# Optimization experiments

Hardware: AMD Instinct MI355X
Metric: run time of the kernel (lower is better)

The kernel has to match this reference:

```python
import jax, jax.numpy as jnp
import numpy as np

DIM = 8          # per-head dim
ATT_EPS = 1e-15
BN_EPS = 1e-6


def setup_inputs() -> dict:
    key = jax.random.key(0)
    ks = jax.random.split(key, 6)
    B, C, H, W = 8, 256, 64, 64
    td = 256                      # heads * dim = 32 * 8
    return {
        'x':      jax.random.normal(ks[0], (B, C, H, W), jnp.float32),
        'w_qkv':  jax.random.normal(ks[1], (3 * td, C), jnp.float32) * 0.05,
        'w_dw':   jax.random.normal(ks[2], (3 * td, 1, 5, 5), jnp.float32) * 0.05,
        'w_pw':   jax.random.normal(ks[3], (96, 8, 8), jnp.float32) * 0.05,   # (groups, out/g, in/g)
        'w_proj': jax.random.normal(ks[4], (C, 2 * td), jnp.float32) * 0.05,
        'bn_gamma': jnp.ones((C,), jnp.float32),
        'bn_beta':  jnp.zeros((C,), jnp.float32),
        'bn_mean':  jnp.zeros((C,), jnp.float32),
        'bn_var':   jnp.ones((C,), jnp.float32),
    }


def _relu_linear_att(ms, H, W):
    # ms: [B, C, H, W] with C = heads * 3*DIM
    B = ms.shape[0]
    d = DIM
    qkv = ms.reshape(B, -1, 3 * d, H * W).transpose(0, 1, 3, 2)   # [B, h, N, 3d]
    q = jax.nn.relu(qkv[..., :d])
    k = jax.nn.relu(qkv[..., d:2 * d])
    v = qkv[..., 2 * d:]
    v = jnp.pad(v, ((0, 0), (0, 0), (0, 0), (0, 1)), constant_values=1.0)  # ones column
    kv = jnp.einsum('bhnd,bhne->bhde', k, v)                       # [B, h, d, d+1]
    out = jnp.einsum('bhnd,bhde->bhne', q, kv)                     # [B, h, N, d+1]
    out = out[..., :-1] / (out[..., -1:] + ATT_EPS)
    return out.transpose(0, 1, 3, 2).reshape(B, -1, H, W)          # [B, h*d, H, W]


def reference(x, w_qkv, w_dw, w_pw, w_proj, bn_gamma, bn_beta, bn_mean, bn_var):
    B, C, H, W = x.shape
    # 1x1 qkv projection
    qkv = jnp.einsum('oc,bchw->bohw', w_qkv, x)                    # [B, 768, H, W]
    # multiscale aggregation: 5x5 depthwise then grouped 1x1 (groups = 3*heads = 96)
    dw = jax.lax.conv_general_dilated(
        qkv, w_dw, window_strides=(1, 1), padding=[(2, 2), (2, 2)],
        dimension_numbers=('NCHW', 'OIHW', 'NCHW'),
        feature_group_count=qkv.shape[1])
    G, O, I = w_pw.shape
    agg = jnp.einsum('goi,bgihw->bgohw', w_pw,
                     dw.reshape(B, G, I, H, W)).reshape(B, G * O, H, W)
    ms = jnp.concatenate([qkv, agg], axis=1)                       # [B, 1536, H, W]
    att = _relu_linear_att(ms, H, W)                               # [B, 512, H, W]
    # proj: 1x1 conv + BatchNorm (eval mode) + identity activation
    p = jnp.einsum('oc,bchw->bohw', w_proj, att)                   # [B, 256, H, W]
    inv = bn_gamma / jnp.sqrt(bn_var + BN_EPS)
    p = p * inv[None, :, None, None] + (bn_beta - bn_mean * inv)[None, :, None, None]
    return x + p
```

## Files before the change

### kernel.cpp

```cpp
#include <hip/hip_runtime.h>
#include <hip/hip_bf16.h>


#define HW 4096
#define ATT_EPS 1e-15f
#define BN_EPS 1e-6f

typedef __attribute__((ext_vector_type(8))) short short8;
typedef __attribute__((ext_vector_type(4))) short short4v;
typedef __attribute__((ext_vector_type(4))) float f32x4;
typedef __attribute__((ext_vector_type(2))) float f32x2;
typedef __attribute__((ext_vector_type(8))) unsigned short u16x8;
typedef __attribute__((ext_vector_type(4))) unsigned short u16x4;

static __device__ inline short f2bf(float f) {
    union { float f; unsigned u; } v; v.f = f;
    unsigned r = v.u + 0x7fff + ((v.u >> 16) & 1);
    return (short)(r >> 16);
}
static __device__ inline float bf2f(unsigned short u) {
    union { unsigned u; float f; } v; v.u = (unsigned)u << 16; return v.f;
}

__global__ __launch_bounds__(256) void prep_w(const float* __restrict__ wproj,
                                              unsigned short* __restrict__ wbf) {
    const int i = (blockIdx.x * 256 + threadIdx.x) * 4;
    float4 v = *(const float4*)&wproj[i];
    u16x4 r = {(unsigned short)f2bf(v.x), (unsigned short)f2bf(v.y),
               (unsigned short)f2bf(v.z), (unsigned short)f2bf(v.w)};
    *(u16x4*)&wbf[i] = r;
}

__global__ __launch_bounds__(256) void qkv_gemm(const float* __restrict__ x,
                                                const float* __restrict__ w,
                                                unsigned short* __restrict__ qkv) {
    __shared__ short A_l[128 * 40];
    __shared__ short B_l[128 * 40];
    const int t  = threadIdx.x;
    const int b  = blockIdx.z;
    const int ob = blockIdx.y * 128;
    const int nb = blockIdx.x * 128;
    const float* xb = x + (size_t)b * 256 * HW;

    const int lane = t & 63, wave = t >> 6;
    const int wo = (wave >> 1) * 64, wn = (wave & 1) * 64;

    f32x4 acc[4][4];
#pragma unroll
    for (int s = 0; s < 4; s++)
#pragma unroll
        for (int u = 0; u < 4; u++) acc[s][u] = (f32x4){0.f, 0.f, 0.f, 0.f};

    const int col4 = (t & 7) * 4;
    const int r0   = t >> 3;
    for (int kb = 0; kb < 256; kb += 32) {
        __syncthreads();
#pragma unroll
        for (int i = 0; i < 4; i++) {
            const int r = r0 + 32 * i;
            float4 v = *(const float4*)&w[(ob + r) * 256 + kb + col4];
            short4v s4 = {f2bf(v.x), f2bf(v.y), f2bf(v.z), f2bf(v.w)};
            *(short4v*)&A_l[r * 40 + col4] = s4;
        }
#pragma unroll
        for (int i = 0; i < 4; i++) {
            const int n4 = (t & 7) + 8 * i;
            float4 v = *(const float4*)&xb[(size_t)(kb + r0) * HW + nb + n4 * 4];
            B_l[(n4 * 4 + 0) * 40 + r0] = f2bf(v.x);
            B_l[(n4 * 4 + 1) * 40 + r0] = f2bf(v.y);
            B_l[(n4 * 4 + 2) * 40 + r0] = f2bf(v.z);
            B_l[(n4 * 4 + 3) * 40 + r0] = f2bf(v.w);
        }
        __syncthreads();

        short8 af[4], bf[4];
#pragma unroll
        for (int s = 0; s < 4; s++)
            af[s] = *(const short8*)&A_l[(wo + s * 16 + (lane & 15)) * 40 + (lane >> 4) * 8];
#pragma unroll
        for (int u = 0; u < 4; u++)
            bf[u] = *(const short8*)&B_l[(wn + u * 16 + (lane & 15)) * 40 + (lane >> 4) * 8];
#pragma unroll
        for (int s = 0; s < 4; s++)
#pragma unroll
            for (int u = 0; u < 4; u++)
                acc[s][u] = __builtin_amdgcn_mfma_f32_16x16x32_bf16(af[s], bf[u], acc[s][u], 0, 0, 0);
    }

#pragma unroll
    for (int s = 0; s < 4; s++)
#pragma unroll
        for (int u = 0; u < 4; u++)
#pragma unroll
            for (int r = 0; r < 4; r++) {
                const int o = ob + wo + s * 16 + (lane >> 4) * 4 + r;
                const int n = nb + wn + u * 16 + (lane & 15);
                qkv[((size_t)b * 768 + o) * HW + n] = (unsigned short)f2bf(acc[s][u][r]);
            }
}

__global__ __launch_bounds__(256, 6) void dw_agg(const unsigned short* __restrict__ qkv,
                                                 const float* __restrict__ wdw,
                                                 const float* __restrict__ wpw,
                                                 unsigned short* __restrict__ agg) {
    __shared__ float tile_raw[8 + 4 * 20 * 64 + 8];
    float* tile = tile_raw + 8;
    const int b = blockIdx.z, g = blockIdx.y;
    const int y0 = blockIdx.x * 16;
    const int t = threadIdx.x;
    const int tx = t & 15, ty = t >> 4;

    const float* wkg = wdw + g * 8 * 25;
    const float* pwg = wpw + g * 64;

    float out[8][4];
#pragma unroll
    for (int o = 0; o < 8; o++)
#pragma unroll
        for (int j = 0; j < 4; j++) out[o][j] = 0.f;

#pragma unroll 1
    for (int half = 0; half < 2; half++) {
        if (half) __syncthreads();
#pragma unroll
        for (int k = 0; k < 3; k++) {
            const int i = t + 256 * k;
            if (i < 640) {
                const int c8 = i & 7, rr = (i >> 3) % 20, ch = i / 160;
                const int y = y0 - 2 + rr;
                u16x8 v = {0, 0, 0, 0, 0, 0, 0, 0};
                if (y >= 0 && y < 64)
                    v = *(const u16x8*)&qkv[((size_t)(b * 768 + g * 8 + half * 4 + ch)) * HW + y * 64 + c8 * 8];
                f32x4 lo = {bf2f(v[0]), bf2f(v[1]), bf2f(v[2]), bf2f(v[3])};
                f32x4 hi = {bf2f(v[4]), bf2f(v[5]), bf2f(v[6]), bf2f(v[7])};
                *(f32x4*)&tile[i * 8]     = lo;
                *(f32x4*)&tile[i * 8 + 4] = hi;
            }
        }
        __syncthreads();

#pragma unroll 1
        for (int ch4 = 0; ch4 < 4; ch4++) {
            const int ch = half * 4 + ch4;
            const float* wkc = wkg + ch * 25;
            float a0 = 0.f, a1 = 0.f, a2 = 0.f, a3 = 0.f;
#pragma unroll
            for (int dy = 0; dy < 5; dy++) {
                const int off = ch4 * 1280 + (ty + dy) * 64 + tx * 4;
                f32x4 C = *(const f32x4*)&tile[off];
                f32x2 L = *(const f32x2*)&tile[off - 2];
                f32x2 R = *(const f32x2*)&tile[off + 4];
                float win[8];
                win[0] = (tx == 0)  ? 0.f : L[0];
                win[1] = (tx == 0)  ? 0.f : L[1];
                win[2] = C[0]; win[3] = C[1];
                win[4] = C[2]; win[5] = C[3];
                win[6] = (tx == 15) ? 0.f : R[0];
                win[7] = (tx == 15) ? 0.f : R[1];
#pragma unroll
                for (int dx = 0; dx < 5; dx++) {
                    const float wv = wkc[dy * 5 + dx];
                    a0 += wv * win[dx + 0];
                    a1 += wv * win[dx + 1];
                    a2 += wv * win[dx + 2];
                    a3 += wv * win[dx + 3];
                }
            }
#pragma unroll
            for (int o = 0; o < 8; o++) {
                const float wv = pwg[o * 8 + ch];
                out[o][0] += wv * a0; out[o][1] += wv * a1;
                out[o][2] += wv * a2; out[o][3] += wv * a3;
            }
        }
    }

#pragma unroll
    for (int o = 0; o < 8; o++) {
        u16x4 rv = {(unsigned short)f2bf(out[o][0]), (unsigned short)f2bf(out[o][1]),
                    (unsigned short)f2bf(out[o][2]), (unsigned short)f2bf(out[o][3])};
        *(u16x4*)&agg[((size_t)(b * 768 + g * 8 + o)) * HW + (y0 + ty) * 64 + tx * 4] = rv;
    }
}

__global__ __launch_bounds__(256) void kv_pass(const unsigned short* __restrict__ qkv,
                                               const unsigned short* __restrict__ agg,
                                               float* __restrict__ kvpart) {
    const int t = threadIdx.x;
    const int w = t >> 6, lane = t & 63;
    const int hp = blockIdx.x * 4 + w;
    const int b = blockIdx.y, c = blockIdx.z;
    const int h0 = hp * 2, h1 = h0 + 1;
    const unsigned short* buf = (h0 < 32) ? qkv : agg;
    const int cb0 = (h0 & 31) * 24, cb1 = (h1 & 31) * 24;

    const int row = lane & 15, kgrp = lane >> 4;
    const int n0 = c * 256 + kgrp * 8;

    const int chA = (row < 8) ? (cb0 + 8 + row) : (cb1 + row);
    const unsigned short* ap = buf + ((size_t)b * 768 + chA) * HW + n0;

    const bool bload = (row < 8);
    const unsigned short* bp0 = buf + ((size_t)b * 768 + cb0 + 16 + (row & 7)) * HW + n0;
    const unsigned short* bp1 = buf + ((size_t)b * 768 + cb1 + 16 + (row & 7)) * HW + n0;
    const short cfill = (row == 8) ? (short)0x3F80 : (short)0;
    const short8 bconst = {cfill, cfill, cfill, cfill, cfill, cfill, cfill, cfill};

    f32x4 acc0 = {0.f, 0.f, 0.f, 0.f};
    f32x4 acc1 = {0.f, 0.f, 0.f, 0.f};

#pragma unroll
    for (int i = 0; i < 8; i++) {
        u16x8 av = *(const u16x8*)(ap + i * 32);
        short8 b0 = bload ? *(const short8*)(bp0 + i * 32) : bconst;
        short8 b1 = bload ? *(const short8*)(bp1 + i * 32) : bconst;
        short8 ar;
#pragma unroll
        for (int j = 0; j < 8; j++)
            ar[j] = (short)((av[j] & 0x8000) ? 0 : av[j]);
        acc0 = __builtin_amdgcn_mfma_f32_16x16x32_bf16(ar, b0, acc0, 0, 0, 0);
        acc1 = __builtin_amdgcn_mfma_f32_16x16x32_bf16(ar, b1, acc1, 0, 0, 0);
    }

    if (row <= 8) {
        float* kp;
        f32x4 a;
        int dbase;
        if (kgrp < 2) {
            kp = kvpart + (size_t)c * 36864 + (size_t)(b * 64 + h0) * 72;
            a = acc0; dbase = kgrp * 4;
        } else {
            kp = kvpart + (size_t)c * 36864 + (size_t)(b * 64 + h1) * 72;
            a = acc1; dbase = (kgrp - 2) * 4;
        }
#pragma unroll
        for (int r = 0; r < 4; r++)
            kp[(dbase + r) * 9 + row] = a[r];
    }
}

__global__ __launch_bounds__(256) void kv_red(const float* __restrict__ kvpart,
                                              float* __restrict__ kvout) {
    const int i = blockIdx.x * 256 + threadIdx.x;
    float s = 0.f;
#pragma unroll
    for (int c = 0; c < 16; c++) s += kvpart[(size_t)c * 36864 + i];
    kvout[i] = s;
}

__global__ __launch_bounds__(256) void att_pass(const unsigned short* __restrict__ qkv,
                                                const unsigned short* __restrict__ agg,
                                                const float* __restrict__ kvbuf,
                                                unsigned short* __restrict__ att_f) {
    const int h = blockIdx.y, b = blockIdx.z;
    const int t = threadIdx.x;
    const float* kvp = kvbuf + ((size_t)(b * 64 + h)) * 72;

    float kvr[72];
#pragma unroll
    for (int i = 0; i < 18; i++) {
        f32x4 v = *(const f32x4*)&kvp[i * 4];
        kvr[i * 4 + 0] = v[0]; kvr[i * 4 + 1] = v[1];
        kvr[i * 4 + 2] = v[2]; kvr[i * 4 + 3] = v[3];
    }

    const unsigned short* buf = (h < 32) ? qkv : agg;
    const int cbase = (h & 31) * 24;
    const int n0 = (blockIdx.x * 256 + t) * 8;
    const unsigned short* qp = buf + ((size_t)b * 768 + cbase) * HW + n0;

    float q[8][8];
#pragma unroll
    for (int d = 0; d < 8; d++) {
        u16x8 v = *(const u16x8*)&qp[(size_t)d * HW];
#pragma unroll
        for (int j = 0; j < 8; j++) q[d][j] = fmaxf(bf2f(v[j]), 0.f);
    }

    unsigned short* op = att_f + (((size_t)(b * 64 + h)) * HW + n0) * 8;
#pragma unroll
    for (int j = 0; j < 8; j++) {
        float num[9];
#pragma unroll
        for (int e = 0; e < 9; e++) num[e] = 0.f;
#pragma unroll
        for (int d = 0; d < 8; d++) {
            const float qv = q[d][j];
#pragma unroll
            for (int e = 0; e < 9; e++) num[e] += qv * kvr[d * 9 + e];
        }
        const float rden = 1.f / (num[8] + ATT_EPS);
        u16x8 r;
#pragma unroll
        for (int e = 0; e < 8; e++) r[e] = (unsigned short)f2bf(num[e] * rden);
        *(u16x8*)&op[j * 8] = r;
    }
}

__global__ __launch_bounds__(256) void proj_gemm(const unsigned short* __restrict__ wbf,
                                                 const unsigned short* __restrict__ att_f,
                                                 const float* __restrict__ gamma,
                                                 const float* __restrict__ beta,
                                                 const float* __restrict__ mean,
                                                 const float* __restrict__ var,
                                                 const float* __restrict__ x,
                                                 float* __restrict__ out) {
    const int t  = threadIdx.x;
    const int b  = blockIdx.z;
    const int ob = blockIdx.y * 128;
    const int nb = blockIdx.x * 128;
    const int lane = t & 63, wave = t >> 6;
    const int wo = (wave >> 1) * 64, wn = (wave & 1) * 64;

    const int am = lane & 15, ak = lane >> 4;
    const unsigned short* ap0 = wbf + (size_t)(ob + wo + am) * 512 + ak * 8;
    const unsigned short* bp0 = att_f +
        (((size_t)b * 64 + ak) * HW + nb + wn + am) * 8;

    f32x4 acc[4][4];
#pragma unroll
    for (int s = 0; s < 4; s++)
#pragma unroll
        for (int u = 0; u < 4; u++) acc[s][u] = (f32x4){0.f, 0.f, 0.f, 0.f};

    for (int kb = 0; kb < 512; kb += 32) {
        short8 af[4], bf[4];
#pragma unroll
        for (int s = 0; s < 4; s++)
            af[s] = *(const short8*)(ap0 + (size_t)s * 16 * 512 + kb);
#pragma unroll
        for (int u = 0; u < 4; u++)
            bf[u] = *(const short8*)(bp0 + ((size_t)(kb >> 3) * HW + u * 16) * 8);
#pragma unroll
        for (int s = 0; s < 4; s++)
#pragma unroll
            for (int u = 0; u < 4; u++)
                acc[s][u] = __builtin_amdgcn_mfma_f32_16x16x32_bf16(af[s], bf[u], acc[s][u], 0, 0, 0);
    }

#pragma unroll
    for (int s = 0; s < 4; s++) {
        const int o_base = ob + wo + s * 16 + (lane >> 4) * 4;
#pragma unroll
        for (int r = 0; r < 4; r++) {
            const int o = o_base + r;
            const float inv = gamma[o] * rsqrtf(var[o] + BN_EPS);
            const float sh  = beta[o] - mean[o] * inv;
#pragma unroll
            for (int u = 0; u < 4; u++) {
                const int n = nb + wn + u * 16 + (lane & 15);
                const size_t idx = ((size_t)b * 256 + o) * HW + n;
                out[idx] = x[idx] + acc[s][u][r] * inv + sh;
            }
        }
    }
}

extern "C" void kernel_launch(void* const* d_in, const int* in_sizes, int n_in,
                              void* d_out, int out_size, void* d_ws, size_t ws_size,
                              hipStream_t stream) {
    const float* x      = (const float*)d_in[0];
    const float* w_qkv  = (const float*)d_in[1];
    const float* w_dw   = (const float*)d_in[2];
    const float* w_pw   = (const float*)d_in[3];
    const float* w_proj = (const float*)d_in[4];
    const float* gamma  = (const float*)d_in[5];
    const float* beta   = (const float*)d_in[6];
    const float* mean   = (const float*)d_in[7];
    const float* var    = (const float*)d_in[8];
    float* out = (float*)d_out;

    unsigned short* qkv  = (unsigned short*)d_ws;
    unsigned short* agg  = qkv + (size_t)25165824;
    unsigned short* attf = agg + (size_t)25165824;
    unsigned short* wbf  = attf + (size_t)16777216;
    float* kvb = (float*)(wbf + (size_t)131072);
    float* kvpart = (float*)attf;

    prep_w  <<<dim3(128),       256, 0, stream>>>(w_proj, wbf);
    qkv_gemm<<<dim3(32, 6, 8),  256, 0, stream>>>(x, w_qkv, qkv);
    dw_agg  <<<dim3(4, 96, 8),  256, 0, stream>>>(qkv, w_dw, w_pw, agg);
    kv_pass <<<dim3(8, 8, 16),  256, 0, stream>>>(qkv, agg, kvpart);
    kv_red  <<<dim3(144),       256, 0, stream>>>(kvpart, kvb);
    att_pass<<<dim3(2, 64, 8),  256, 0, stream>>>(qkv, agg, kvb, attf);
    proj_gemm<<<dim3(32, 2, 8), 256, 0, stream>>>(wbf, attf,
                                                  gamma, beta, mean, var, x, out);
}
```

Before: 220.8 us.

## Pre-convert qkv weights to bf16 and load A fragments directly from global

Adds a prep kernel that converts w_qkv to bf16 once into a scratch area of the attention buffer. The qkv GEMM then reads A fragments straight from global memory into registers, dropping the A shared-memory tile. The x tile is now loaded as per-column scalar reads along K, with each thread packing 8 bf16 values into one 16-byte LDS store instead of scattered 2-byte stores. This aims to cut LDS traffic and repeated conversion work, at the cost of one extra launch and strided scalar global loads.

```diff
diff --git a/kernel.cpp b/kernel.cpp
--- a/kernel.cpp
+++ b/kernel.cpp
@@ -31,19 +31,33 @@
     *(u16x4*)&wbf[i] = r;
 }
 
+__global__ __launch_bounds__(256) void prep_wq(const float* __restrict__ wqkv,
+                                               unsigned short* __restrict__ wqbf) {
+    const int i = (blockIdx.x * 256 + threadIdx.x) * 4;
+    float4 v = *(const float4*)&wqkv[i];
+    u16x4 r = {(unsigned short)f2bf(v.x), (unsigned short)f2bf(v.y),
+               (unsigned short)f2bf(v.z), (unsigned short)f2bf(v.w)};
+    *(u16x4*)&wqbf[i] = r;
+}
+
 __global__ __launch_bounds__(256) void qkv_gemm(const float* __restrict__ x,
-                                                const float* __restrict__ w,
+                                                const unsigned short* __restrict__ wqbf,
                                                 unsigned short* __restrict__ qkv) {
-    __shared__ short A_l[128 * 40];
-    __shared__ short B_l[128 * 40];
+    __shared__ unsigned short B_l[128 * 40];
     const int t  = threadIdx.x;
     const int b  = blockIdx.z;
     const int ob = blockIdx.y * 128;
     const int nb = blockIdx.x * 128;
-    const float* xb = x + (size_t)b * 256 * HW;
 
     const int lane = t & 63, wave = t >> 6;
     const int wo = (wave >> 1) * 64, wn = (wave & 1) * 64;
+    const int am = lane & 15, ak = lane >> 4;
+
+    const unsigned short* ap0 = wqbf + (size_t)(ob + wo + am) * 256 + ak * 8;
+
+    const int n   = t & 127;
+    const int kg0 = t >> 7;
+    const float* xb = x + (size_t)b * 256 * HW + nb + n;
 
     f32x4 acc[4][4];
 #pragma unroll
@@ -51,35 +65,30 @@
 #pragma unroll
         for (int u = 0; u < 4; u++) acc[s][u] = (f32x4){0.f, 0.f, 0.f, 0.f};
 
-    const int col4 = (t & 7) * 4;
-    const int r0   = t >> 3;
     for (int kb = 0; kb < 256; kb += 32) {
+        short8 af[4];
+#pragma unroll
+        for (int s = 0; s < 4; s++)
+            af[s] = *(const short8*)(ap0 + (size_t)s * 16 * 256 + kb);
+
         __syncthreads();
 #pragma unroll
-        for (int i = 0; i < 4; i++) {
-            const int r = r0 + 32 * i;
-            float4 v = *(const float4*)&w[(ob + r) * 256 + kb + col4];
-            short4v s4 = {f2bf(v.x), f2bf(v.y), f2bf(v.z), f2bf(v.w)};
-            *(short4v*)&A_l[r * 40 + col4] = s4;
-        }
-#pragma unroll
-        for (int i = 0; i < 4; i++) {
-            const int n4 = (t & 7) + 8 * i;
-            float4 v = *(const float4*)&xb[(size_t)(kb + r0) * HW + nb + n4 * 4];
-            B_l[(n4 * 4 + 0) * 40 + r0] = f2bf(v.x);
-            B_l[(n4 * 4 + 1) * 40 + r0] = f2bf(v.y);
-            B_l[(n4 * 4 + 2) * 40 + r0] = f2bf(v.z);
-            B_l[(n4 * 4 + 3) * 40 + r0] = f2bf(v.w);
+        for (int q = 0; q < 2; q++) {
+            const int kg = kg0 + q * 2;
+            u16x8 pk;
+#pragma unroll
+            for (int j = 0; j < 8; j++) {
+                float v = xb[(size_t)(kb + kg * 8 + j) * HW];
+                pk[j] = (unsigned short)f2bf(v);
+            }
+            *(u16x8*)&B_l[n * 40 + kg * 8] = pk;
         }
         __syncthreads();
 
-        short8 af[4], bf[4];
-#pragma unroll
-        for (int s = 0; s < 4; s++)
-            af[s] = *(const short8*)&A_l[(wo + s * 16 + (lane & 15)) * 40 + (lane >> 4) * 8];
+        short8 bf[4];
 #pragma unroll
         for (int u = 0; u < 4; u++)
-            bf[u] = *(const short8*)&B_l[(wn + u * 16 + (lane & 15)) * 40 + (lane >> 4) * 8];
+            bf[u] = *(const short8*)&B_l[(wn + u * 16 + am) * 40 + ak * 8];
 #pragma unroll
         for (int s = 0; s < 4; s++)
 #pragma unroll
@@ -94,8 +103,8 @@
 #pragma unroll
             for (int r = 0; r < 4; r++) {
                 const int o = ob + wo + s * 16 + (lane >> 4) * 4 + r;
-                const int n = nb + wn + u * 16 + (lane & 15);
-                qkv[((size_t)b * 768 + o) * HW + n] = (unsigned short)f2bf(acc[s][u][r]);
+                const int nn = nb + wn + u * 16 + (lane & 15);
+                qkv[((size_t)b * 768 + o) * HW + nn] = (unsigned short)f2bf(acc[s][u][r]);
             }
 }
 
@@ -376,9 +385,11 @@
     unsigned short* wbf  = attf + (size_t)16777216;
     float* kvb = (float*)(wbf + (size_t)131072);
     float* kvpart = (float*)attf;
+    unsigned short* wqbf = attf + (size_t)4194304;
 
     prep_w  <<<dim3(128),       256, 0, stream>>>(w_proj, wbf);
-    qkv_gemm<<<dim3(32, 6, 8),  256, 0, stream>>>(x, w_qkv, qkv);
+    prep_wq <<<dim3(192),       256, 0, stream>>>(w_qkv, wqbf);
+    qkv_gemm<<<dim3(32, 6, 8),  256, 0, stream>>>(x, wqbf, qkv);
     dw_agg  <<<dim3(4, 96, 8),  256, 0, stream>>>(qkv, w_dw, w_pw, agg);
     kv_pass <<<dim3(8, 8, 16),  256, 0, stream>>>(qkv, agg, kvpart);
     kv_red  <<<dim3(144),       256, 0, stream>>>(kvpart, kvb);
```

New measurement: 227.3 us. 1.03x slower.
